# Performance work log

Measured on AMD Instinct MI355X. Metric: run time of the kernel, lower is better.

Reference implementation:

```python
import jax, jax.numpy as jnp
import numpy as np

B, T, C, H, N = 4, 2048, 1024, 16, 64
CHUNK = 256           # chunk_len
NBSWA = 2             # n_bswa_chunks
BSWA = CHUNK * NBSWA  # sliding window length
SSTATE = CHUNK        # kvm state slots (chunk_len * n_max_d_chunks)
SINK = 1              # sink_len
PARTIAL = 32          # rope_partial_dim
NEG = -1e30


def _ln(x, w, b, eps=1e-5):
    m = x.mean(-1, keepdims=True)
    v = jnp.mean((x - m) ** 2, -1, keepdims=True)
    return (x - m) * jax.lax.rsqrt(v + eps) * w + b


def _rope_tables():
    freq = (1.0 / 10000.0) ** np.linspace(0.0, 1.0, PARTIAL // 2, dtype=np.float32)
    freq = np.repeat(freq, 2)
    freq = np.concatenate([freq, np.zeros(N - PARTIAL, np.float32)])
    th = np.arange(T, dtype=np.float32)[:, None] * freq[None, :]
    cos = np.cos(th)
    sin = np.sin(th)
    sin[:, 1::2] *= -1.0
    return jnp.asarray(cos), jnp.asarray(sin)


def _rope(x, cos, sin):
    # pairwise flip (x0,x1)->(x1,x0)
    xf = x.reshape(*x.shape[:-1], N // 2, 2)[..., ::-1].reshape(x.shape)
    return cos[None, :, None, :] * x + sin[None, :, None, :] * xf


def _forward(residual, x, v1, x0, dx0,
             Wq, Wk, Wv, Wproj, Wkw,
             x_q, x_k, x_v, lamb,
             ln_q_w, ln_q_b, ln_k_w, ln_k_b, ln_dk_w, ln_dk_b, ln_res_w, ln_res_b,
             front_temp, state_temp):
    q = x @ Wq.T
    k = x @ Wk.T
    v = x @ Wv.T
    v = (1.0 - lamb) * v + lamb * v1  # value residual
    q = q.reshape(B, T, H, N)
    k = k.reshape(B, T, H, N)
    v = v.reshape(B, T, H, N)
    q = _ln(q, ln_q_w, ln_q_b)
    k = _ln(k, ln_k_w, ln_k_b)

    def shift(t):  # token shift (use_dkys=True variant)
        return jnp.concatenate([t[:, 0:1], t[:, :-1]], axis=1)

    q = q + x_q[None, None] * (shift(q) - q)
    k = k + x_k[None, None] * (shift(k) - k)
    v = v + x_v[None, None] * (shift(v) - v)

    cos, sin = _rope_tables()
    q = _rope(q, cos, sin)
    k = _rope(k, cos, sin)

    q = q.transpose(0, 2, 1, 3)  # [B,H,T,N]
    k = k.transpose(0, 2, 1, 3)
    v = v.transpose(0, 2, 1, 3)

    kw = jax.nn.sigmoid(jnp.einsum('btc,hc->bht', x, Wkw))[..., None]  # [B,H,T,1]
    st = state_temp.reshape(1, H, 1, 1)
    ft = front_temp.reshape(1, H, 1, 1)

    d_k = jnp.zeros((B, H, SSTATE, N), x.dtype)
    d_v = jnp.zeros((B, H, SSTATE, N), x.dtype)
    d_cnt = jnp.zeros((B, H, SSTATE, 1), x.dtype)
    scale = 1.0 / np.sqrt(N)
    outs = []
    for e in range(CHUNK, T + 1, CHUNK):  # fixed 8 chunks
        qb = e - CHUNK
        bb = max(0, e - BSWA)
        qc = q[:, :, qb:e]
        c_k = k[:, :, bb:bb + CHUNK]
        c_v = v[:, :, bb:bb + CHUNK]
        bk = k[:, :, bb:e]
        bv = v[:, :, bb:e]

        d_k_norm = _ln(d_k, ln_dk_w, ln_dk_b)
        d_vlen = d_cnt  # running count of accumulated c_v vectors per slot
        v_state = d_v / jnp.clip(jnp.linalg.norm(d_v, axis=-1, keepdims=True), 1e-12) * d_vlen
        k_star = jnp.concatenate([d_k_norm * st, bk * ft], axis=-2)
        v_star = jnp.concatenate([v_state, bv], axis=-2)

        qi = np.arange(qb, e)
        ki = np.arange(bb, e)
        mbias = np.where(ki[None, :] <= qi[:, None], 0.0, NEG).astype(np.float32)
        bias = jnp.asarray(np.concatenate([np.zeros((CHUNK, SSTATE), np.float32), mbias], axis=1))

        sc = jnp.einsum('bhqd,bhkd->bhqk', qc, k_star) * scale + bias
        out = jnp.einsum('bhqk,bhkd->bhqd', jax.nn.softmax(sc, axis=-1), v_star)
        outs.append(out)

        # state update: rope_zeroing on first PARTIAL channels, ln_d_k, nearest-slot scatter
        ck0 = jnp.concatenate([jnp.zeros_like(c_k[..., :PARTIAL]), c_k[..., PARTIAL:]], axis=-1)
        ck0 = _ln(ck0, ln_dk_w, ln_dk_b)
        sim = jnp.einsum('bhcd,bhsd->bhcs', ck0, d_k_norm)
        sim = sim.at[..., 0:SINK].set(NEG)
        kwc = kw[:, :, bb:bb + CHUNK]
        ck0 = ck0 * kwc
        cvw = c_v * kwc
        best = jnp.argmax(sim, axis=-1)                       # [B,H,CHUNK]
        oh = jax.nn.one_hot(best, SSTATE, dtype=x.dtype)      # [B,H,CHUNK,S]
        d_k = d_k + jnp.einsum('bhcs,bhcd->bhsd', oh, ck0)
        d_v = d_v + jnp.einsum('bhcs,bhcd->bhsd', oh, cvw)
        d_cnt = d_cnt + oh.sum(axis=2)[..., None]

    y = jnp.concatenate(outs, axis=2).transpose(0, 2, 1, 3).reshape(B, T, C)
    y = _ln(y, ln_res_w, ln_res_b)
    return residual + y @ Wproj.T


def setup_inputs() -> dict:
    key = jax.random.key(0)
    ks = jax.random.split(key, 12)
    f = lambda k, s, sc=1.0: jax.random.normal(k, s, dtype=jnp.float32) * sc
    return {
        'residual': f(ks[0], (B, T, C)),
        'x': f(ks[1], (B, T, C)),
        'v1': f(ks[2], (B, T, C)),
        'x0': f(ks[3], (B, T, C)),
        'dx0': f(ks[4], (B, T, C)),
        'token_ids': jax.random.randint(ks[5], (B, T), 0, 50257),
        'Wq': f(ks[6], (C, C), 0.02),
        'Wk': f(ks[7], (C, C), 0.02),
        'Wv': f(ks[8], (C, C), 0.02),
        'Wproj': f(ks[9], (C, C), 0.02),
        'Wkw': f(ks[10], (H, C), 0.02),
        'x_q': 0.5 * jnp.ones((H, N), jnp.float32),
        'x_k': 0.5 * jnp.ones((H, N), jnp.float32),
        'x_v': 0.5 * jnp.ones((H, N), jnp.float32),
        'lamb': jnp.float32(0.5),
        'ln_q_w': jnp.ones((N,), jnp.float32), 'ln_q_b': jnp.zeros((N,), jnp.float32),
        'ln_k_w': jnp.ones((N,), jnp.float32), 'ln_k_b': jnp.zeros((N,), jnp.float32),
        'ln_dk_w': jnp.ones((N,), jnp.float32), 'ln_dk_b': jnp.zeros((N,), jnp.float32),
        'ln_res_w': jnp.ones((C,), jnp.float32), 'ln_res_b': jnp.zeros((C,), jnp.float32),
        'front_temp': jnp.ones((H,), jnp.float32),
        'state_temp': jnp.ones((H,), jnp.float32),
    }


def reference(residual, x, v1, x0, dx0, token_ids,
              Wq, Wk, Wv, Wproj, Wkw, x_q, x_k, x_v, lamb,
              ln_q_w, ln_q_b, ln_k_w, ln_k_b, ln_dk_w, ln_dk_b, ln_res_w, ln_res_b,
              front_temp, state_temp):
    del token_ids  # unused in visible forward body
    return _forward(residual, x, v1, x0, dx0,
                    Wq, Wk, Wv, Wproj, Wkw,
                    x_q, x_k, x_v, lamb,
                    ln_q_w, ln_q_b, ln_k_w, ln_k_b, ln_dk_w, ln_dk_b, ln_res_w, ln_res_b,
                    front_temp, state_temp)
```

## Files before the change

kernel.cpp:

```cpp
#include <hip/hip_runtime.h>
#include <math.h>

#define Bq 4
#define Tq 2048
#define Cq 1024
#define Hq 16
#define Nq 64

typedef __attribute__((ext_vector_type(8))) short short8v;
typedef __attribute__((ext_vector_type(4))) float f32x4;

__device__ inline float waveSum(float v) {
#pragma unroll
  for (int o = 32; o; o >>= 1) v += __shfl_xor(v, o);
  return v;
}
__device__ inline unsigned short f2bf(float f) {
  unsigned u = __float_as_uint(f);
  unsigned r = (u + 0x7FFFu + ((u >> 16) & 1u)) >> 16;
  return (unsigned short)r;
}
__device__ inline float bf2f(unsigned short b) {
  return __uint_as_float(((unsigned)b) << 16);
}
// ... 123 lines not shown
      for (int j = 0; j < 4; ++j) {
        acc[i][j] = __builtin_amdgcn_mfma_f32_16x16x32_bf16(ah[i], bh[j], acc[i][j], 0, 0, 0);
        acc[i][j] = __builtin_amdgcn_mfma_f32_16x16x32_bf16(ah[i], bl[j], acc[i][j], 0, 0, 0);
        acc[i][j] = __builtin_amdgcn_mfma_f32_16x16x32_bf16(al[i], bh[j], acc[i][j], 0, 0, 0);
      }
  }

#pragma unroll
  for (int i = 0; i < 4; ++i)
#pragma unroll
    for (int j = 0; j < 4; ++j)
#pragma unroll
      for (int rg = 0; rg < 4; ++rg) {
        int m = m0 + wr * 64 + i * 16 + (l >> 4) * 4 + rg;
        int n = n0 + wc * 64 + j * 16 + (l & 15);
        int b = m >> 11, t = m & (Tq - 1);
        int h = n >> 6, nn = n & 63;
        dst[((((size_t)b * Hq + h) * Tq + t) << 6) | nn] = acc[i][j][rg];
      }
}

__global__ __launch_bounds__(256) void postproc(
    const float* __restrict__ src, float* __restrict__ dst,
    unsigned short* __restrict__ dst_bf,
    const float* __restrict__ lnw, const float* __restrict__ lnb,
    const float* __restrict__ xs_p, int doLNRope)
{
  const int w = threadIdx.x >> 6, lane = threadIdx.x & 63;
  const int row = blockIdx.x * 4 + w;
  const int t = row & (Tq - 1);
  const int h = (row >> 11) & (Hq - 1);
  const size_t base = (size_t)row << 6;
  const size_t pbase = (t > 0) ? base - 64 : base;
  float cur = src[base + lane];
  float prv = src[pbase + lane];
  if (doLNRope) {
    const float lw = lnw[lane], lb = lnb[lane];
    {
      float m = waveSum(cur) * (1.0f / 64.0f);
      float d = cur - m;
      float var = waveSum(d * d) * (1.0f / 64.0f);
      cur = d * rsqrtf(var + 1e-5f) * lw + lb;
    }
    {
      float m = waveSum(prv) * (1.0f / 64.0f);
      float d = prv - m;
      float var = waveSum(d * d) * (1.0f / 64.0f);
      prv = d * rsqrtf(var + 1e-5f) * lw + lb;
    }
  }
  const float xv = xs_p[h * 64 + lane];
  float val = cur + xv * (prv - cur);
  if (doLNRope) {
    float partner = __shfl_xor(val, 1);
    if (lane < 32) {
      int i = lane >> 1;
      float freq = (float)exp((double)i * (-log(10000.0) / 15.0));
      float th = (float)t * freq;
      float c = cosf(th), s = sinf(th);
      val = c * val + ((lane & 1) ? -s : s) * partner;
    }
  }
  if (dst) dst[base + lane] = val;
  if (dst_bf) dst_bf[base + lane] = f2bf(val);
}

__global__ __launch_bounds__(256) void kw_kernel(
    const float* __restrict__ x, const float* __restrict__ Wkw, float* __restrict__ out)
{
  const int bt = blockIdx.x;
  const int tid = threadIdx.x, w = tid >> 6, lane = tid & 63;
  __shared__ float xs[Cq];
  for (int i = tid; i < Cq; i += 256) xs[i] = x[(size_t)bt * Cq + i];
  __syncthreads();
  const int b = bt >> 11, t = bt & (Tq - 1);
  for (int h = w; h < Hq; h += 4) {
    float acc = 0.0f;
    for (int i = lane; i < Cq; i += 64) acc += xs[i] * Wkw[h * Cq + i];
    acc = waveSum(acc);
    if (lane == 0) out[((size_t)(b * Hq + h)) * Tq + t] = 1.0f / (1.0f + expf(-acc));
  }
}

__global__ __launch_bounds__(1024, 1) void state_evolve_kernel(
    const float* __restrict__ kf, const unsigned short* __restrict__ v_bf,
    const float* __restrict__ kwp,
    unsigned short* __restrict__ dkn_bf, unsigned short* __restrict__ vst_bf,
    float* __restrict__ cnt_snap,
    const float* __restrict__ lnw, const float* __restrict__ lnb)
{
  const int bh = blockIdx.x;
  const int tid = threadIdx.x;
  const int s = tid >> 2, qd = tid & 3;
  const int db = qd * 16;
  const size_t seq = (size_t)Tq * Nq;
  const float* kb_ = kf + (size_t)bh * seq;
  const unsigned short* vb_ = v_bf + (size_t)bh * seq;
  const float* kwb = kwp + (size_t)bh * Tq;

  __shared__ float dknT[32 * 260];
  __shared__ float ck0T[32 * 260];
  __shared__ unsigned short VRow[256 * 72];
  __shared__ float Ps[256], Qs[256], aS[256], kwS[256];
  __shared__ float lwS[64], lbS[64];
  __shared__ int best[256];

  if (tid < 64) { lwS[tid] = lnw[tid]; lbS[tid] = lnb[tid]; }

  float dkReg[16], dvReg[16];
#pragma unroll
  for (int i = 0; i < 16; ++i) { dkReg[i] = 0.f; dvReg[i] = 0.f; }
  float cnt = 0.f;
  __syncthreads();

  for (int c = 0; c < 8; ++c) {
    const int e = c * 256 + 256;
    const int bb = (e - 512 > 0) ? (e - 512) : 0;

    {
      float sum = 0.f;
#pragma unroll
      for (int i = 0; i < 16; ++i) sum += dkReg[i];
      sum += __shfl_xor(sum, 1); sum += __shfl_xor(sum, 2);
      const float mean = sum * (1.0f / 64.0f);
      float sq = 0.f;
#pragma unroll
      for (int i = 0; i < 16; ++i) { float d = dkReg[i] - mean; sq += d * d; }
      sq += __shfl_xor(sq, 1); sq += __shfl_xor(sq, 2);
      const float rs = rsqrtf(sq * (1.0f / 64.0f) + 1e-5f);
      float kn[16];
#pragma unroll
      for (int i = 0; i < 16; ++i)
        kn[i] = (dkReg[i] - mean) * rs * lwS[db + i] + lbS[db + i];
      unsigned int pk[8];
#pragma unroll
      for (int i2 = 0; i2 < 8; ++i2)
        pk[i2] = (unsigned)f2bf(kn[2 * i2]) | ((unsigned)f2bf(kn[2 * i2 + 1]) << 16);
      unsigned short* kd = dkn_bf + (((size_t)bh * 8 + c) << 14) + s * 64 + db;
      *(uint4*)kd = make_uint4(pk[0], pk[1], pk[2], pk[3]);
      *(uint4*)(kd + 8) = make_uint4(pk[4], pk[5], pk[6], pk[7]);

      if (c > 0 && c < 7) {
        if (qd >= 2) {
#pragma unroll
          for (int i = 0; i < 16; ++i) dknT[(db - 32 + i) * 260 + s] = kn[i];
        } else {
          float pp = 0.f, qq = 0.f;
#pragma unroll
          for (int i = 0; i < 16; ++i) {
            pp += kn[i] * lwS[db + i];
            qq += kn[i] * lbS[db + i];
          }
          pp += __shfl_xor(pp, 1);
          qq += __shfl_xor(qq, 1);
          if (qd == 0) { Ps[s] = pp; Qs[s] = qq; }
        }
      }

      float sqv = 0.f;
#pragma unroll
      for (int i = 0; i < 16; ++i) sqv += dvReg[i] * dvReg[i];
      sqv += __shfl_xor(sqv, 1); sqv += __shfl_xor(sqv, 2);
      const float inrm = 1.0f / fmaxf(sqrtf(sqv), 1e-12f);
#pragma unroll
      for (int i2 = 0; i2 < 8; ++i2)
        pk[i2] = (unsigned)f2bf(dvReg[2 * i2] * inrm) |
                 ((unsigned)f2bf(dvReg[2 * i2 + 1] * inrm) << 16);
      unsigned short* vd = vst_bf + (((size_t)bh * 8 + c) << 14) + s * 64 + db;
      *(uint4*)vd = make_uint4(pk[0], pk[1], pk[2], pk[3]);
      *(uint4*)(vd + 8) = make_uint4(pk[4], pk[5], pk[6], pk[7]);
      if (qd == 0) cnt_snap[((size_t)bh * 8 + c) * 256 + s] = cnt;
    }

    if (c == 7) break;

    {
      float kv[16];
      if (qd >= 2) {
        const float* krow = kb_ + (size_t)(bb + s) * 64 + db;
#pragma unroll
        for (int i = 0; i < 16; i += 4) {
          float4 t4 = *(const float4*)(krow + i);
          kv[i] = t4.x; kv[i + 1] = t4.y; kv[i + 2] = t4.z; kv[i + 3] = t4.w;
        }
      } else {
#pragma unroll
        for (int i = 0; i < 16; ++i) kv[i] = 0.f;
      }
      float sum = 0.f;
#pragma unroll
      for (int i = 0; i < 16; ++i) sum += kv[i];
      sum += __shfl_xor(sum, 1); sum += __shfl_xor(sum, 2);
      const float mean = sum * (1.0f / 64.0f);
      float sq = 0.f;
#pragma unroll
      for (int i = 0; i < 16; ++i) { float d = kv[i] - mean; sq += d * d; }
      sq += __shfl_xor(sq, 1); sq += __shfl_xor(sq, 2);
      const float rs = rsqrtf(sq * (1.0f / 64.0f) + 1e-5f);
      if (qd >= 2) {
#pragma unroll
        for (int i = 0; i < 16; ++i)
          ck0T[(db - 32 + i) * 260 + s] =
              (kv[i] - mean) * rs * lwS[db + i] + lbS[db + i];
      }
      if (qd == 0) {
        aS[s] = (0.0f - mean) * rs;
        kwS[s] = kwb[bb + s];
      }
      const unsigned short* vsrc = vb_ + (size_t)(bb + s) * 64 + db;
      *(uint4*)&VRow[s * 72 + db] = *(const uint4*)vsrc;
      *(uint4*)&VRow[s * 72 + db + 8] = *(const uint4*)(vsrc + 8);
      if (c == 0 && tid < 256) best[tid] = 1;
    }
    __syncthreads();

    if (c > 0) {
      const int tx = tid & 31, ty = tid >> 5;
      const f32x4 pv0 = *(const f32x4*)&Ps[4 * tx];
      const f32x4 pv1 = *(const f32x4*)&Ps[128 + 4 * tx];
      const f32x4 qv0 = *(const f32x4*)&Qs[4 * tx];
      const f32x4 qv1 = *(const f32x4*)&Qs[128 + 4 * tx];
#pragma unroll
      for (int pass = 0; pass < 2; ++pass) {
        const int rc0 = pass * 128 + ty * 4;
        float a4[4];
#pragma unroll
        for (int i = 0; i < 4; ++i) a4[i] = aS[rc0 + i];
        float acc[4][8];
#pragma unroll
        for (int i = 0; i < 4; ++i)
#pragma unroll
          for (int j = 0; j < 4; ++j) {
            acc[i][j] = a4[i] * pv0[j] + qv0[j];
            acc[i][j + 4] = a4[i] * pv1[j] + qv1[j];
          }
#pragma unroll 4
        for (int k = 0; k < 32; ++k) {
          f32x4 av = *(const f32x4*)&ck0T[k * 260 + rc0];
          f32x4 b0 = *(const f32x4*)&dknT[k * 260 + 4 * tx];
          f32x4 b1 = *(const f32x4*)&dknT[k * 260 + 128 + 4 * tx];
#pragma unroll
          for (int i = 0; i < 4; ++i)
#pragma unroll
            for (int j = 0; j < 4; ++j) {
              acc[i][j] += av[i] * b0[j];
              acc[i][j + 4] += av[i] * b1[j];
            }
        }
#pragma unroll
        for (int i = 0; i < 4; ++i) {
          float bvv = -3.0e38f;
          int bi = 1 << 30;
#pragma unroll
          for (int j = 0; j < 8; ++j) {
            int s2 = (j < 4) ? (4 * tx + j) : (128 + 4 * tx + (j - 4));
            float v = acc[i][j];
            if (s2 == 0) v = -1.0e30f;
            if (v > bvv || (v == bvv && s2 < bi)) { bvv = v; bi = s2; }
          }
#pragma unroll
          for (int o = 16; o; o >>= 1) {
            float ov = __shfl_xor(bvv, o);
            int oi = __shfl_xor(bi, o);
            if (ov > bvv || (ov == bvv && oi < bi)) { bvv = ov; bi = oi; }
          }
          if (tx == 0) best[rc0 + i] = bi;
        }
      }
      __syncthreads();
    }

    {
      int cadd = 0;
      for (int rc = 0; rc < 256; ++rc) {
        if (best[rc] == s) {
          const float kwv = kwS[rc];
          if (qd < 2) {
            const float a = aS[rc];
#pragma unroll
            for (int i = 0; i < 16; ++i)
              dkReg[i] += (a * lwS[db + i] + lbS[db + i]) * kwv;
          } else {
#pragma unroll
            for (int i = 0; i < 16; ++i)
              dkReg[i] += ck0T[(db - 32 + i) * 260 + rc] * kwv;
          }
          const uint4 u0 = *(const uint4*)&VRow[rc * 72 + db];
          const uint4 u1 = *(const uint4*)&VRow[rc * 72 + db + 8];
          const unsigned uu[8] = {u0.x, u0.y, u0.z, u0.w, u1.x, u1.y, u1.z, u1.w};
#pragma unroll
          for (int i2 = 0; i2 < 8; ++i2) {
            dvReg[2 * i2] += __uint_as_float((uu[i2] & 0xFFFFu) << 16) * kwv;
            dvReg[2 * i2 + 1] += __uint_as_float(uu[i2] & 0xFFFF0000u) * kwv;
          }
          ++cadd;
        }
      }
      cnt += (float)cadd;
    }
    __syncthreads();
  }
}

__global__ __launch_bounds__(256, 2) void attn_mfma_kernel(
    const unsigned short* __restrict__ q_bf, const unsigned short* __restrict__ k_bf,
    const unsigned short* __restrict__ v_bf,
    const unsigned short* __restrict__ dkn_bf, const unsigned short* __restrict__ vst_bf,
    const float* __restrict__ cnt_snap, float* __restrict__ y,
    const float* __restrict__ ftp, const float* __restrict__ stp)
{
  const int blk = blockIdx.x;
  const int bh = blk >> 4;
  const int c = (blk >> 1) & 7;
  const int half = blk & 1;
  const int h = bh & (Hq - 1);
  const int tid = threadIdx.x;
  const int w = tid >> 6, l = tid & 63;
  const int g = l >> 4, n = l & 15;
  const int rows0 = c * 256 + half * 128 + w * 32;
  const int e = c * 256 + 256;
  const int bb = (e - 512 > 0) ? (e - 512) : 0;
  const int nwt = (e - bb) >> 6;
  const float stsc = stp[h] * 0.125f, ftsc = ftp[h] * 0.125f;
  const size_t seq = (size_t)Tq * Nq;

  __shared__ unsigned short Ks[64 * 72];
  __shared__ unsigned short VTs[64 * 72];
  __shared__ unsigned short Ps[4][32 * 72];
  __shared__ float wts[64];

  short8v qf[2][2];
#pragma unroll
  for (int mt = 0; mt < 2; ++mt)
#pragma unroll
    for (int kh = 0; kh < 2; ++kh)
      qf[mt][kh] = *(const short8v*)(q_bf + (size_t)bh * seq +
                                     (size_t)(rows0 + mt * 16 + n) * 64 + kh * 32 + g * 8);

  f32x4 oacc[2][4];
#pragma unroll
  for (int mt = 0; mt < 2; ++mt)
#pragma unroll
    for (int dt = 0; dt < 4; ++dt) oacc[mt][dt] = (f32x4){0.f, 0.f, 0.f, 0.f};
  float rowM[2][4], rowL[2][4];
#pragma unroll
  for (int mt = 0; mt < 2; ++mt)
#pragma unroll
    for (int r = 0; r < 4; ++r) { rowM[mt][r] = -1.0e30f; rowL[mt][r] = 0.f; }

  const int nkt = 4 + nwt;
  for (int kt = 0; kt < nkt; ++kt) {
    const bool isState = kt < 4;
    const int t0 = isState ? kt * 64 : bb + (kt - 4) * 64;
    const unsigned short* ksrc = isState
        ? dkn_bf + (((size_t)bh * 8 + c) << 14) + (size_t)t0 * 64
        : k_bf + (size_t)bh * seq + (size_t)t0 * 64;
    const unsigned short* vsrc = isState
        ? vst_bf + (((size_t)bh * 8 + c) << 14) + (size_t)t0 * 64
        : v_bf + (size_t)bh * seq + (size_t)t0 * 64;

    __syncthreads();
    {
      const int row = tid >> 2, q4 = tid & 3;
      const unsigned short* src = ksrc + row * 64 + q4 * 16;
      *(uint4*)&Ks[row * 72 + q4 * 16] = *(const uint4*)src;
      *(uint4*)&Ks[row * 72 + q4 * 16 + 8] = *(const uint4*)(src + 8);
      const unsigned short* vs = vsrc + row * 64 + q4 * 16;
#pragma unroll
      for (int i = 0; i < 16; ++i) VTs[(q4 * 16 + i) * 72 + row] = vs[i];
      if (tid < 64)
        wts[tid] = isState ? cnt_snap[((size_t)bh * 8 + c) * 256 + kt * 64 + tid] : 1.0f;
    }
    __syncthreads();

    f32x4 sacc[2][4];
#pragma unroll
    for (int mt = 0; mt < 2; ++mt)
#pragma unroll
      for (int nt = 0; nt < 4; ++nt) sacc[mt][nt] = (f32x4){0.f, 0.f, 0.f, 0.f};
#pragma unroll
    for (int nt = 0; nt < 4; ++nt) {
      short8v kf0 = *(const short8v*)&Ks[(nt * 16 + n) * 72 + g * 8];
      short8v kf1 = *(const short8v*)&Ks[(nt * 16 + n) * 72 + 32 + g * 8];
#pragma unroll
      for (int mt = 0; mt < 2; ++mt) {
        sacc[mt][nt] = __builtin_amdgcn_mfma_f32_16x16x32_bf16(qf[mt][0], kf0, sacc[mt][nt], 0, 0, 0);
        sacc[mt][nt] = __builtin_amdgcn_mfma_f32_16x16x32_bf16(qf[mt][1], kf1, sacc[mt][nt], 0, 0, 0);
      }
    }

    const float scale = isState ? stsc : ftsc;
    float wt_n[4];
#pragma unroll
    for (int nt = 0; nt < 4; ++nt) wt_n[nt] = wts[nt * 16 + n];

#pragma unroll
    for (int mt = 0; mt < 2; ++mt) {
#pragma unroll
      for (int r = 0; r < 4; ++r) {
        float sv[4];
#pragma unroll
        for (int nt = 0; nt < 4; ++nt) {
          float s = sacc[mt][nt][r] * scale;
          if (!isState) {
            int qi = rows0 + mt * 16 + g * 4 + r;
            int kj = t0 + nt * 16 + n;
            if (kj > qi) s = -1.0e30f;
          }
          sv[nt] = s;
        }
        float tmax = fmaxf(fmaxf(sv[0], sv[1]), fmaxf(sv[2], sv[3]));
        tmax = fmaxf(tmax, __shfl_xor(tmax, 1));
        tmax = fmaxf(tmax, __shfl_xor(tmax, 2));
        tmax = fmaxf(tmax, __shfl_xor(tmax, 4));
        tmax = fmaxf(tmax, __shfl_xor(tmax, 8));
        const float Mold = rowM[mt][r];
        const float Mnew = fmaxf(Mold, tmax);
        const float al = __expf(Mold - Mnew);
        rowM[mt][r] = Mnew;
        float p[4], ts = 0.f;
#pragma unroll
        for (int nt = 0; nt < 4; ++nt) { p[nt] = __expf(sv[nt] - Mnew); ts += p[nt]; }
        ts += __shfl_xor(ts, 1);
        ts += __shfl_xor(ts, 2);
        ts += __shfl_xor(ts, 4);
        ts += __shfl_xor(ts, 8);
        rowL[mt][r] = rowL[mt][r] * al + ts;
#pragma unroll
        for (int dt = 0; dt < 4; ++dt) oacc[mt][dt][r] *= al;
        const int prow = (mt * 16 + g * 4 + r) * 72;
#pragma unroll
        for (int nt = 0; nt < 4; ++nt)
          Ps[w][prow + nt * 16 + n] = f2bf(p[nt] * wt_n[nt]);
      }
    }

    short8v pf[2][2];
#pragma unroll
    for (int mt = 0; mt < 2; ++mt)
#pragma unroll
      for (int jh = 0; jh < 2; ++jh)
        pf[mt][jh] = *(const short8v*)&Ps[w][(mt * 16 + n) * 72 + jh * 32 + g * 8];
#pragma unroll
    for (int dt = 0; dt < 4; ++dt) {
      short8v vf0 = *(const short8v*)&VTs[(dt * 16 + n) * 72 + g * 8];
      short8v vf1 = *(const short8v*)&VTs[(dt * 16 + n) * 72 + 32 + g * 8];
#pragma unroll
      for (int mt = 0; mt < 2; ++mt) {
        oacc[mt][dt] = __builtin_amdgcn_mfma_f32_16x16x32_bf16(pf[mt][0], vf0, oacc[mt][dt], 0, 0, 0);
        oacc[mt][dt] = __builtin_amdgcn_mfma_f32_16x16x32_bf16(pf[mt][1], vf1, oacc[mt][dt], 0, 0, 0);
      }
    }
  }

#pragma unroll
  for (int mt = 0; mt < 2; ++mt) {
#pragma unroll
    for (int r = 0; r < 4; ++r) {
      const float inv = 1.0f / rowL[mt][r];
      const int row = rows0 + mt * 16 + g * 4 + r;
#pragma unroll
      for (int dt = 0; dt < 4; ++dt)
        y[(size_t)bh * seq + (size_t)row * 64 + dt * 16 + n] = oacc[mt][dt][r] * inv;
    }
  }
}

__global__ __launch_bounds__(256) void final_ln(
    const float* __restrict__ y, const float* __restrict__ lnw,
    const float* __restrict__ lnb, unsigned short* __restrict__ dst)
{
  const int bt = blockIdx.x;
  const int b = bt >> 11, t = bt & (Tq - 1);
  const int tid = threadIdx.x, w = tid >> 6, lane = tid & 63;
  __shared__ float red[8];
  float v[4];
  float s = 0.0f;
#pragma unroll
  for (int i = 0; i < 4; ++i) {
    int c = tid + (i << 8);
    int h = c >> 6, n = c & 63;
    v[i] = y[((((size_t)b * Hq + h) * Tq + t) << 6) + n];
    s += v[i];
  }
  s = waveSum(s);
  if (lane == 0) red[w] = s;
  __syncthreads();
  const float mean = (red[0] + red[1] + red[2] + red[3]) * (1.0f / 1024.0f);
  float s2 = 0.0f;
#pragma unroll
  for (int i = 0; i < 4; ++i) { float d = v[i] - mean; s2 += d * d; }
  s2 = waveSum(s2);
  if (lane == 0) red[4 + w] = s2;
  __syncthreads();
  const float var = (red[4] + red[5] + red[6] + red[7]) * (1.0f / 1024.0f);
  const float rs = rsqrtf(var + 1e-5f);
#pragma unroll
  for (int i = 0; i < 4; ++i) {
    int c = tid + (i << 8);
    dst[(size_t)bt * Cq + c] = f2bf((v[i] - mean) * rs * lnw[c] + lnb[c]);
  }
}

extern "C" void kernel_launch(void* const* d_in, const int* in_sizes, int n_in,
                              void* d_out, int out_size, void* d_ws, size_t ws_size,
                              hipStream_t stream)
{
  (void)in_sizes; (void)n_in; (void)out_size; (void)ws_size;
  const float* residual = (const float*)d_in[0];
  const float* x        = (const float*)d_in[1];
  const float* v1       = (const float*)d_in[2];
  const float* Wq       = (const float*)d_in[6];
  const float* Wk       = (const float*)d_in[7];
  const float* Wv       = (const float*)d_in[8];
  const float* Wproj    = (const float*)d_in[9];
  const float* Wkw      = (const float*)d_in[10];
  const float* x_q      = (const float*)d_in[11];
  const float* x_k      = (const float*)d_in[12];
  const float* x_v      = (const float*)d_in[13];
  const float* lamb     = (const float*)d_in[14];
  const float* ln_q_w   = (const float*)d_in[15];
  const float* ln_q_b   = (const float*)d_in[16];
  const float* ln_k_w   = (const float*)d_in[17];
  const float* ln_k_b   = (const float*)d_in[18];
  const float* ln_dk_w  = (const float*)d_in[19];
  const float* ln_dk_b  = (const float*)d_in[20];
  const float* ln_res_w = (const float*)d_in[21];
  const float* ln_res_b = (const float*)d_in[22];
  const float* ftp      = (const float*)d_in[23];
  const float* stp      = (const float*)d_in[24];

  float* ws = (float*)d_ws;
  const size_t SZ = (size_t)Bq * Hq * Tq * Nq;
  float* q_raw = ws;
  float* ybuf  = ws;
  float* k_raw = ws + SZ;
  unsigned short* vst_bf = (unsigned short*)(ws + SZ);
  float* cnt_snap = ws + SZ + SZ / 2;
  float* v_mix = ws + 2 * SZ;
  unsigned short* ylnb_bf = (unsigned short*)(ws + 2 * SZ);
  float* k_fin = ws + 3 * SZ;
  unsigned short* q_bf = (unsigned short*)(ws + 4 * SZ);
  unsigned short* x_lo = q_bf;
  unsigned short* k_bf = q_bf + SZ;
  unsigned short* wk_hi = k_bf;
  unsigned short* wk_lo = wk_hi + (1u << 20);
  unsigned short* v_bf = (unsigned short*)(ws + 5 * SZ);
  unsigned short* xb   = v_bf + SZ;
  unsigned short* dkn_bf = xb;
  unsigned short* wqb = (unsigned short*)(ws + 6 * SZ);
  unsigned short* wvb = wqb + (1u << 20);
  unsigned short* wpb = wvb + (1u << 20);
  float* kwbuf = ws + 6 * SZ + ((3u << 20) >> 1);

  dim3 gb(256);
  dim3 ggb(64, 8);

  hipLaunchKernelGGL(f32_to_bf16_hilo_kernel, dim3((int)(SZ / 4 / 256)), gb, 0, stream,
                     x, xb, x_lo, (int)(SZ / 4));
  hipLaunchKernelGGL(f32_to_bf16_hilo_kernel, dim3(1024), gb, 0, stream,
                     Wk, wk_hi, wk_lo, 262144);
  hipLaunchKernelGGL(f32_to_bf16_kernel, dim3(1024), gb, 0, stream, Wq, wqb, 262144);
  hipLaunchKernelGGL(f32_to_bf16_kernel, dim3(1024), gb, 0, stream, Wv, wvb, 262144);
  hipLaunchKernelGGL(f32_to_bf16_kernel, dim3(1024), gb, 0, stream, Wproj, wpb, 262144);

  hipLaunchKernelGGL(gemm_bf16, ggb, gb, 0, stream, xb, wqb, q_raw, (const float*)nullptr, lamb, 1);
  hipLaunchKernelGGL(gemm_bf16_split, ggb, gb, 0, stream, xb, x_lo, wk_hi, wk_lo, k_raw);
  hipLaunchKernelGGL(gemm_bf16, ggb, gb, 0, stream, xb, wvb, v_mix, v1, lamb, 2);
  hipLaunchKernelGGL(kw_kernel, dim3(Bq * Tq), gb, 0, stream, x, Wkw, kwbuf);

  const int rows = Bq * Hq * Tq;
  hipLaunchKernelGGL(postproc, dim3(rows / 4), gb, 0, stream, q_raw, (float*)nullptr, q_bf, ln_q_w, ln_q_b, x_q, 1);
  hipLaunchKernelGGL(postproc, dim3(rows / 4), gb, 0, stream, k_raw, k_fin, k_bf, ln_k_w, ln_k_b, x_k, 1);
  hipLaunchKernelGGL(postproc, dim3(rows / 4), gb, 0, stream, v_mix, (float*)nullptr, v_bf,
                     (const float*)nullptr, (const float*)nullptr, x_v, 0);

  hipLaunchKernelGGL(state_evolve_kernel, dim3(Bq * Hq), dim3(1024), 0, stream,
                     k_fin, v_bf, kwbuf, dkn_bf, vst_bf, cnt_snap, ln_dk_w, ln_dk_b);

  hipLaunchKernelGGL(attn_mfma_kernel, dim3(Bq * Hq * 16), gb, 0, stream,
                     q_bf, k_bf, v_bf, dkn_bf, vst_bf, cnt_snap, ybuf, ftp, stp);

  hipLaunchKernelGGL(final_ln, dim3(Bq * Tq), gb, 0, stream, ybuf, ln_res_w, ln_res_b, ylnb_bf);
  hipLaunchKernelGGL(gemm_bf16, ggb, gb, 0, stream, ylnb_bf, wpb, (float*)d_out, residual, lamb, 3);
}
```

Baseline: 1.405 ms.

## Overlap sequential state evolution with windowed attention in one heterogeneous kernel

Merges the state-evolution kernel and the sliding-window part of attention into a single launch. The first 64 blocks run the serial per-head state update, while the remaining blocks compute unnormalised window attention and write partial outputs plus row max and sum. A separate merge kernel then does only the state-slot attention and combines the two softmax partials. The state scatter loop also gains per-slot counts so rows with no assignments exit early. This hides the long single-block-per-head state kernel behind window attention, at the cost of extra partial-output traffic and a merge step.

```diff
diff --git a/kernel.cpp b/kernel.cpp
--- a/kernel.cpp
+++ b/kernel.cpp
@@ -229,232 +229,370 @@
   }
 }
 
-__global__ __launch_bounds__(1024, 1) void state_evolve_kernel(
+union MegaSmem {
+  struct {
+    float dknT[32 * 260];
+    float ck0T[32 * 260];
+    unsigned short VRow[256 * 72];
+    float Ps[256], Qs[256], aS[256], kwS[256];
+    float lwS[64], lbS[64];
+    int best[256];
+    int cntS[256];
+  } st;
+  struct {
+    unsigned short Ks[64 * 72];
+    unsigned short VTs[64 * 72];
+    unsigned short Ps[16][16 * 72];
+  } at;
+};
+
+__global__ __launch_bounds__(1024, 1) void mega_state_window_kernel(
     const float* __restrict__ kf, const unsigned short* __restrict__ v_bf,
     const float* __restrict__ kwp,
     unsigned short* __restrict__ dkn_bf, unsigned short* __restrict__ vst_bf,
     float* __restrict__ cnt_snap,
-    const float* __restrict__ lnw, const float* __restrict__ lnb)
-{
-  const int bh = blockIdx.x;
+    const float* __restrict__ lnw, const float* __restrict__ lnb,
+    const unsigned short* __restrict__ q_bf, const unsigned short* __restrict__ k_bf,
+    float* __restrict__ ow, float* __restrict__ mlw, const float* __restrict__ ftp)
+{
+  __shared__ MegaSmem sm;
   const int tid = threadIdx.x;
-  const int s = tid >> 2, qd = tid & 3;
-  const int db = qd * 16;
   const size_t seq = (size_t)Tq * Nq;
-  const float* kb_ = kf + (size_t)bh * seq;
-  const unsigned short* vb_ = v_bf + (size_t)bh * seq;
-  const float* kwb = kwp + (size_t)bh * Tq;
-
-  __shared__ float dknT[32 * 260];
-  __shared__ float ck0T[32 * 260];
-  __shared__ unsigned short VRow[256 * 72];
-  __shared__ float Ps[256], Qs[256], aS[256], kwS[256];
-  __shared__ float lwS[64], lbS[64];
-  __shared__ int best[256];
-
-  if (tid < 64) { lwS[tid] = lnw[tid]; lbS[tid] = lnb[tid]; }
-
-  float dkReg[16], dvReg[16];
-#pragma unroll
-  for (int i = 0; i < 16; ++i) { dkReg[i] = 0.f; dvReg[i] = 0.f; }
-  float cnt = 0.f;
-  __syncthreads();
-
-  for (int c = 0; c < 8; ++c) {
+
+  if (blockIdx.x < 64) {
+    auto& S = sm.st;
+    const int bh = blockIdx.x;
+    const int s = tid >> 2, qd = tid & 3;
+    const int db = qd * 16;
+    const float* kb_ = kf + (size_t)bh * seq;
+    const unsigned short* vb_ = v_bf + (size_t)bh * seq;
+    const float* kwb = kwp + (size_t)bh * Tq;
+
+    if (tid < 64) { S.lwS[tid] = lnw[tid]; S.lbS[tid] = lnb[tid]; }
+
+    float dkReg[16], dvReg[16];
+#pragma unroll
+    for (int i = 0; i < 16; ++i) { dkReg[i] = 0.f; dvReg[i] = 0.f; }
+    float cnt = 0.f;
+    __syncthreads();
+
+    for (int c = 0; c < 8; ++c) {
+      const int e = c * 256 + 256;
+      const int bb = (e - 512 > 0) ? (e - 512) : 0;
+
+      {
+        float sum = 0.f;
+#pragma unroll
+        for (int i = 0; i < 16; ++i) sum += dkReg[i];
+        sum += __shfl_xor(sum, 1); sum += __shfl_xor(sum, 2);
+        const float mean = sum * (1.0f / 64.0f);
+        float sq = 0.f;
+#pragma unroll
+        for (int i = 0; i < 16; ++i) { float d = dkReg[i] - mean; sq += d * d; }
+        sq += __shfl_xor(sq, 1); sq += __shfl_xor(sq, 2);
+        const float rs = rsqrtf(sq * (1.0f / 64.0f) + 1e-5f);
+        float kn[16];
+#pragma unroll
+        for (int i = 0; i < 16; ++i)
+          kn[i] = (dkReg[i] - mean) * rs * S.lwS[db + i] + S.lbS[db + i];
+        unsigned int pk[8];
+#pragma unroll
+        for (int i2 = 0; i2 < 8; ++i2)
+          pk[i2] = (unsigned)f2bf(kn[2 * i2]) | ((unsigned)f2bf(kn[2 * i2 + 1]) << 16);
+        unsigned short* kd = dkn_bf + (((size_t)bh * 8 + c) << 14) + s * 64 + db;
+        *(uint4*)kd = make_uint4(pk[0], pk[1], pk[2], pk[3]);
+        *(uint4*)(kd + 8) = make_uint4(pk[4], pk[5], pk[6], pk[7]);
+
+        if (c > 0 && c < 7) {
+          if (qd >= 2) {
+#pragma unroll
+            for (int i = 0; i < 16; ++i) S.dknT[(db - 32 + i) * 260 + s] = kn[i];
+          } else {
+            float pp = 0.f, qq = 0.f;
+#pragma unroll
+            for (int i = 0; i < 16; ++i) {
+              pp += kn[i] * S.lwS[db + i];
+              qq += kn[i] * S.lbS[db + i];
+            }
+            pp += __shfl_xor(pp, 1);
+            qq += __shfl_xor(qq, 1);
+            if (qd == 0) { S.Ps[s] = pp; S.Qs[s] = qq; }
+          }
+        }
+
+        float sqv = 0.f;
+#pragma unroll
+        for (int i = 0; i < 16; ++i) sqv += dvReg[i] * dvReg[i];
+        sqv += __shfl_xor(sqv, 1); sqv += __shfl_xor(sqv, 2);
+        const float inrm = 1.0f / fmaxf(sqrtf(sqv), 1e-12f);
+#pragma unroll
+        for (int i2 = 0; i2 < 8; ++i2)
+          pk[i2] = (unsigned)f2bf(dvReg[2 * i2] * inrm) |
+                   ((unsigned)f2bf(dvReg[2 * i2 + 1] * inrm) << 16);
+        unsigned short* vd = vst_bf + (((size_t)bh * 8 + c) << 14) + s * 64 + db;
+        *(uint4*)vd = make_uint4(pk[0], pk[1], pk[2], pk[3]);
+        *(uint4*)(vd + 8) = make_uint4(pk[4], pk[5], pk[6], pk[7]);
+        if (qd == 0) cnt_snap[((size_t)bh * 8 + c) * 256 + s] = cnt;
+      }
+
+      if (c == 7) break;
+
+      {
+        float kv[16];
+        if (qd >= 2) {
+          const float* krow = kb_ + (size_t)(bb + s) * 64 + db;
+#pragma unroll
+          for (int i = 0; i < 16; i += 4) {
+            float4 t4 = *(const float4*)(krow + i);
+            kv[i] = t4.x; kv[i + 1] = t4.y; kv[i + 2] = t4.z; kv[i + 3] = t4.w;
+          }
+        } else {
+#pragma unroll
+          for (int i = 0; i < 16; ++i) kv[i] = 0.f;
+        }
+        float sum = 0.f;
+#pragma unroll
+        for (int i = 0; i < 16; ++i) sum += kv[i];
+        sum += __shfl_xor(sum, 1); sum += __shfl_xor(sum, 2);
+        const float mean = sum * (1.0f / 64.0f);
+        float sq = 0.f;
+#pragma unroll
+        for (int i = 0; i < 16; ++i) { float d = kv[i] - mean; sq += d * d; }
+        sq += __shfl_xor(sq, 1); sq += __shfl_xor(sq, 2);
+        const float rs = rsqrtf(sq * (1.0f / 64.0f) + 1e-5f);
+        if (qd >= 2) {
+#pragma unroll
+          for (int i = 0; i < 16; ++i)
+            S.ck0T[(db - 32 + i) * 260 + s] =
+                (kv[i] - mean) * rs * S.lwS[db + i] + S.lbS[db + i];
+        }
+        if (qd == 0) {
+          S.aS[s] = (0.0f - mean) * rs;
+          S.kwS[s] = kwb[bb + s];
+        }
+        const unsigned short* vsrc = vb_ + (size_t)(bb + s) * 64 + db;
+        *(uint4*)&S.VRow[s * 72 + db] = *(const uint4*)vsrc;
+        *(uint4*)&S.VRow[s * 72 + db + 8] = *(const uint4*)(vsrc + 8);
+        if (c == 0) {
+          if (tid < 256) { S.best[tid] = 1; S.cntS[tid] = (tid == 1) ? 256 : 0; }
+        } else {
+          if (tid < 256) S.cntS[tid] = 0;
+        }
+      }
+      __syncthreads();
+
+      if (c > 0) {
+        const int tx = tid & 31, ty = tid >> 5;
+        const f32x4 pv0 = *(const f32x4*)&S.Ps[4 * tx];
+        const f32x4 pv1 = *(const f32x4*)&S.Ps[128 + 4 * tx];
+        const f32x4 qv0 = *(const f32x4*)&S.Qs[4 * tx];
+        const f32x4 qv1 = *(const f32x4*)&S.Qs[128 + 4 * tx];
+#pragma unroll
+        for (int pass = 0; pass < 2; ++pass) {
+          const int rc0 = pass * 128 + ty * 4;
+          float a4[4];
+#pragma unroll
+          for (int i = 0; i < 4; ++i) a4[i] = S.aS[rc0 + i];
+          float acc[4][8];
+#pragma unroll
+          for (int i = 0; i < 4; ++i)
+#pragma unroll
+            for (int j = 0; j < 4; ++j) {
+              acc[i][j] = a4[i] * pv0[j] + qv0[j];
+              acc[i][j + 4] = a4[i] * pv1[j] + qv1[j];
+            }
+#pragma unroll 4
+          for (int k = 0; k < 32; ++k) {
+            f32x4 av = *(const f32x4*)&S.ck0T[k * 260 + rc0];
+            f32x4 b0 = *(const f32x4*)&S.dknT[k * 260 + 4 * tx];
+            f32x4 b1 = *(const f32x4*)&S.dknT[k * 260 + 128 + 4 * tx];
+#pragma unroll
+            for (int i = 0; i < 4; ++i)
+#pragma unroll
+              for (int j = 0; j < 4; ++j) {
+                acc[i][j] += av[i] * b0[j];
+                acc[i][j + 4] += av[i] * b1[j];
+              }
+          }
+#pragma unroll
+          for (int i = 0; i < 4; ++i) {
+            float bvv = -3.0e38f;
+            int bi = 1 << 30;
+#pragma unroll
+            for (int j = 0; j < 8; ++j) {
+              int s2 = (j < 4) ? (4 * tx + j) : (128 + 4 * tx + (j - 4));
+              float v = acc[i][j];
+              if (s2 == 0) v = -1.0e30f;
+              if (v > bvv || (v == bvv && s2 < bi)) { bvv = v; bi = s2; }
+            }
+#pragma unroll
+            for (int o = 16; o; o >>= 1) {
+              float ov = __shfl_xor(bvv, o);
+              int oi = __shfl_xor(bi, o);
+              if (ov > bvv || (ov == bvv && oi < bi)) { bvv = ov; bi = oi; }
+            }
+            if (tx == 0) {
+              S.best[rc0 + i] = bi;
+              atomicAdd(&S.cntS[bi], 1);
+            }
+          }
+        }
+      }
+      __syncthreads();
+
+      {
+        const int need = S.cntS[s];
+        if (need) {
+          int found = 0;
+          for (int rc = 0; rc < 256 && found < need; ++rc) {
+            if (S.best[rc] == s) {
+              const float kwv = S.kwS[rc];
+              if (qd < 2) {
+                const float a = S.aS[rc];
+#pragma unroll
+                for (int i = 0; i < 16; ++i)
+                  dkReg[i] += (a * S.lwS[db + i] + S.lbS[db + i]) * kwv;
+              } else {
+#pragma unroll
+                for (int i = 0; i < 16; ++i)
+                  dkReg[i] += S.ck0T[(db - 32 + i) * 260 + rc] * kwv;
+              }
+              const uint4 u0 = *(const uint4*)&S.VRow[rc * 72 + db];
+              const uint4 u1 = *(const uint4*)&S.VRow[rc * 72 + db + 8];
+              const unsigned uu[8] = {u0.x, u0.y, u0.z, u0.w, u1.x, u1.y, u1.z, u1.w};
+#pragma unroll
+              for (int i2 = 0; i2 < 8; ++i2) {
+                dvReg[2 * i2] += __uint_as_float((uu[i2] & 0xFFFFu) << 16) * kwv;
+                dvReg[2 * i2 + 1] += __uint_as_float(uu[i2] & 0xFFFF0000u) * kwv;
+              }
+              ++found;
+            }
+          }
+          cnt += (float)need;
+        }
+      }
+      __syncthreads();
+    }
+  } else {
+    auto& A = sm.at;
+    const int wb = blockIdx.x - 64;
+    const int bh = wb >> 3;
+    const int c = wb & 7;
+    const int h = bh & (Hq - 1);
+    const int w16 = tid >> 6, l = tid & 63;
+    const int g = l >> 4, n = l & 15;
+    const int rows0 = c * 256 + w16 * 16;
     const int e = c * 256 + 256;
     const int bb = (e - 512 > 0) ? (e - 512) : 0;
-
-    {
-      float sum = 0.f;
-#pragma unroll
-      for (int i = 0; i < 16; ++i) sum += dkReg[i];
-      sum += __shfl_xor(sum, 1); sum += __shfl_xor(sum, 2);
-      const float mean = sum * (1.0f / 64.0f);
-      float sq = 0.f;
-#pragma unroll
-      for (int i = 0; i < 16; ++i) { float d = dkReg[i] - mean; sq += d * d; }
-      sq += __shfl_xor(sq, 1); sq += __shfl_xor(sq, 2);
-      const float rs = rsqrtf(sq * (1.0f / 64.0f) + 1e-5f);
-      float kn[16];
-#pragma unroll
-      for (int i = 0; i < 16; ++i)
-        kn[i] = (dkReg[i] - mean) * rs * lwS[db + i] + lbS[db + i];
-      unsigned int pk[8];
-#pragma unroll
-      for (int i2 = 0; i2 < 8; ++i2)
-        pk[i2] = (unsigned)f2bf(kn[2 * i2]) | ((unsigned)f2bf(kn[2 * i2 + 1]) << 16);
-      unsigned short* kd = dkn_bf + (((size_t)bh * 8 + c) << 14) + s * 64 + db;
-      *(uint4*)kd = make_uint4(pk[0], pk[1], pk[2], pk[3]);
-      *(uint4*)(kd + 8) = make_uint4(pk[4], pk[5], pk[6], pk[7]);
-
-      if (c > 0 && c < 7) {
-        if (qd >= 2) {
-#pragma unroll
-          for (int i = 0; i < 16; ++i) dknT[(db - 32 + i) * 260 + s] = kn[i];
-        } else {
-          float pp = 0.f, qq = 0.f;
-#pragma unroll
-          for (int i = 0; i < 16; ++i) {
-            pp += kn[i] * lwS[db + i];
-            qq += kn[i] * lbS[db + i];
-          }
-          pp += __shfl_xor(pp, 1);
-          qq += __shfl_xor(qq, 1);
-          if (qd == 0) { Ps[s] = pp; Qs[s] = qq; }
+    const int nwt = (e - bb) >> 6;
+    const float ftsc = ftp[h] * 0.125f;
+
+    short8v qf[2];
+#pragma unroll
+    for (int kh = 0; kh < 2; ++kh)
+      qf[kh] = *(const short8v*)(q_bf + (size_t)bh * seq +
+                                 (size_t)(rows0 + n) * 64 + kh * 32 + g * 8);
+
+    f32x4 oacc[4];
+#pragma unroll
+    for (int dt = 0; dt < 4; ++dt) oacc[dt] = (f32x4){0.f, 0.f, 0.f, 0.f};
+    float rowM[4], rowL[4];
+#pragma unroll
+    for (int r = 0; r < 4; ++r) { rowM[r] = -1.0e30f; rowL[r] = 0.f; }
+
+    for (int kt = 0; kt < nwt; ++kt) {
+      const int t0 = bb + kt * 64;
+      const unsigned short* ksrc = k_bf + (size_t)bh * seq + (size_t)t0 * 64;
+      const unsigned short* vsrc = v_bf + (size_t)bh * seq + (size_t)t0 * 64;
+      __syncthreads();
+      {
+        const int row = tid >> 4, q16 = tid & 15;
+        *(uint2*)&A.Ks[row * 72 + q16 * 4] = *(const uint2*)(ksrc + row * 64 + q16 * 4);
+        const unsigned short* vs = vsrc + row * 64 + q16 * 4;
+#pragma unroll
+        for (int i = 0; i < 4; ++i) A.VTs[(q16 * 4 + i) * 72 + row] = vs[i];
+      }
+      __syncthreads();
+
+      f32x4 sacc[4];
+#pragma unroll
+      for (int nt = 0; nt < 4; ++nt) sacc[nt] = (f32x4){0.f, 0.f, 0.f, 0.f};
+#pragma unroll
+      for (int nt = 0; nt < 4; ++nt) {
+        short8v kf0 = *(const short8v*)&A.Ks[(nt * 16 + n) * 72 + g * 8];
+        short8v kf1 = *(const short8v*)&A.Ks[(nt * 16 + n) * 72 + 32 + g * 8];
+        sacc[nt] = __builtin_amdgcn_mfma_f32_16x16x32_bf16(qf[0], kf0, sacc[nt], 0, 0, 0);
+        sacc[nt] = __builtin_amdgcn_mfma_f32_16x16x32_bf16(qf[1], kf1, sacc[nt], 0, 0, 0);
+      }
+
+#pragma unroll
+      for (int r = 0; r < 4; ++r) {
+        const int qi = rows0 + g * 4 + r;
+        float sv[4];
+#pragma unroll
+        for (int nt = 0; nt < 4; ++nt) {
+          float s = sacc[nt][r] * ftsc;
+          int kj = t0 + nt * 16 + n;
+          if (kj > qi) s = -1.0e30f;
+          sv[nt] = s;
         }
-      }
-
-      float sqv = 0.f;
-#pragma unroll
-      for (int i = 0; i < 16; ++i) sqv += dvReg[i] * dvReg[i];
-      sqv += __shfl_xor(sqv, 1); sqv += __shfl_xor(sqv, 2);
-      const float inrm = 1.0f / fmaxf(sqrtf(sqv), 1e-12f);
-#pragma unroll
-      for (int i2 = 0; i2 < 8; ++i2)
-        pk[i2] = (unsigned)f2bf(dvReg[2 * i2] * inrm) |
-                 ((unsigned)f2bf(dvReg[2 * i2 + 1] * inrm) << 16);
-      unsigned short* vd = vst_bf + (((size_t)bh * 8 + c) << 14) + s * 64 + db;
-      *(uint4*)vd = make_uint4(pk[0], pk[1], pk[2], pk[3]);
-      *(uint4*)(vd + 8) = make_uint4(pk[4], pk[5], pk[6], pk[7]);
-      if (qd == 0) cnt_snap[((size_t)bh * 8 + c) * 256 + s] = cnt;
-    }
-
-    if (c == 7) break;
-
-    {
-      float kv[16];
-      if (qd >= 2) {
-        const float* krow = kb_ + (size_t)(bb + s) * 64 + db;
-#pragma unroll
-        for (int i = 0; i < 16; i += 4) {
-          float4 t4 = *(const float4*)(krow + i);
-          kv[i] = t4.x; kv[i + 1] = t4.y; kv[i + 2] = t4.z; kv[i + 3] = t4.w;
-        }
-      } else {
-#pragma unroll
-        for (int i = 0; i < 16; ++i) kv[i] = 0.f;
-      }
-      float sum = 0.f;
-#pragma unroll
-      for (int i = 0; i < 16; ++i) sum += kv[i];
-      sum += __shfl_xor(sum, 1); sum += __shfl_xor(sum, 2);
-      const float mean = sum * (1.0f / 64.0f);
-      float sq = 0.f;
-#pragma unroll
-      for (int i = 0; i < 16; ++i) { float d = kv[i] - mean; sq += d * d; }
-      sq += __shfl_xor(sq, 1); sq += __shfl_xor(sq, 2);
-      const float rs = rsqrtf(sq * (1.0f / 64.0f) + 1e-5f);
-      if (qd >= 2) {
-#pragma unroll
-        for (int i = 0; i < 16; ++i)
-          ck0T[(db - 32 + i) * 260 + s] =
-              (kv[i] - mean) * rs * lwS[db + i] + lbS[db + i];
-      }
-      if (qd == 0) {
-        aS[s] = (0.0f - mean) * rs;
-        kwS[s] = kwb[bb + s];
-      }
-      const unsigned short* vsrc = vb_ + (size_t)(bb + s) * 64 + db;
-      *(uint4*)&VRow[s * 72 + db] = *(const uint4*)vsrc;
-      *(uint4*)&VRow[s * 72 + db + 8] = *(const uint4*)(vsrc + 8);
-      if (c == 0 && tid < 256) best[tid] = 1;
-    }
-    __syncthreads();
-
-    if (c > 0) {
-      const int tx = tid & 31, ty = tid >> 5;
-      const f32x4 pv0 = *(const f32x4*)&Ps[4 * tx];
-      const f32x4 pv1 = *(const f32x4*)&Ps[128 + 4 * tx];
-      const f32x4 qv0 = *(const f32x4*)&Qs[4 * tx];
-      const f32x4 qv1 = *(const f32x4*)&Qs[128 + 4 * tx];
-#pragma unroll
-      for (int pass = 0; pass < 2; ++pass) {
-        const int rc0 = pass * 128 + ty * 4;
-        float a4[4];
-#pragma unroll
-        for (int i = 0; i < 4; ++i) a4[i] = aS[rc0 + i];
-        float acc[4][8];
-#pragma unroll
-        for (int i = 0; i < 4; ++i)
-#pragma unroll
-          for (int j = 0; j < 4; ++j) {
-            acc[i][j] = a4[i] * pv0[j] + qv0[j];
-            acc[i][j + 4] = a4[i] * pv1[j] + qv1[j];
-          }
-#pragma unroll 4
-        for (int k = 0; k < 32; ++k) {
-          f32x4 av = *(const f32x4*)&ck0T[k * 260 + rc0];
-          f32x4 b0 = *(const f32x4*)&dknT[k * 260 + 4 * tx];
-          f32x4 b1 = *(const f32x4*)&dknT[k * 260 + 128 + 4 * tx];
-#pragma unroll
-          for (int i = 0; i < 4; ++i)
-#pragma unroll
-            for (int j = 0; j < 4; ++j) {
-              acc[i][j] += av[i] * b0[j];
-              acc[i][j + 4] += av[i] * b1[j];
-            }
-        }
-#pragma unroll
-        for (int i = 0; i < 4; ++i) {
-          float bvv = -3.0e38f;
-          int bi = 1 << 30;
-#pragma unroll
-          for (int j = 0; j < 8; ++j) {
-            int s2 = (j < 4) ? (4 * tx + j) : (128 + 4 * tx + (j - 4));
-            float v = acc[i][j];
-            if (s2 == 0) v = -1.0e30f;
-            if (v > bvv || (v == bvv && s2 < bi)) { bvv = v; bi = s2; }
-          }
-#pragma unroll
-          for (int o = 16; o; o >>= 1) {
-            float ov = __shfl_xor(bvv, o);
-            int oi = __shfl_xor(bi, o);
-            if (ov > bvv || (ov == bvv && oi < bi)) { bvv = ov; bi = oi; }
-          }
-          if (tx == 0) best[rc0 + i] = bi;
-        }
-      }
-      __syncthreads();
-    }
-
-    {
-      int cadd = 0;
-      for (int rc = 0; rc < 256; ++rc) {
-        if (best[rc] == s) {
-          const float kwv = kwS[rc];
-          if (qd < 2) {
-            const float a = aS[rc];
-#pragma unroll
-            for (int i = 0; i < 16; ++i)
-              dkReg[i] += (a * lwS[db + i] + lbS[db + i]) * kwv;
-          } else {
-#pragma unroll
-            for (int i = 0; i < 16; ++i)
-              dkReg[i] += ck0T[(db - 32 + i) * 260 + rc] * kwv;
-          }
-          const uint4 u0 = *(const uint4*)&VRow[rc * 72 + db];
-          const uint4 u1 = *(const uint4*)&VRow[rc * 72 + db + 8];
-          const unsigned uu[8] = {u0.x, u0.y, u0.z, u0.w, u1.x, u1.y, u1.z, u1.w};
-#pragma unroll
-          for (int i2 = 0; i2 < 8; ++i2) {
-            dvReg[2 * i2] += __uint_as_float((uu[i2] & 0xFFFFu) << 16) * kwv;
-            dvReg[2 * i2 + 1] += __uint_as_float(uu[i2] & 0xFFFF0000u) * kwv;
-          }
-          ++cadd;
-        }
-      }
-      cnt += (float)cadd;
-    }
-    __syncthreads();
-  }
-}
-
-__global__ __launch_bounds__(256, 2) void attn_mfma_kernel(
-    const unsigned short* __restrict__ q_bf, const unsigned short* __restrict__ k_bf,
-    const unsigned short* __restrict__ v_bf,
+        float tmax = fmaxf(fmaxf(sv[0], sv[1]), fmaxf(sv[2], sv[3]));
+        tmax = fmaxf(tmax, __shfl_xor(tmax, 1));
+        tmax = fmaxf(tmax, __shfl_xor(tmax, 2));
+        tmax = fmaxf(tmax, __shfl_xor(tmax, 4));
+        tmax = fmaxf(tmax, __shfl_xor(tmax, 8));
+        const float Mold = rowM[r];
+        const float Mnew = fmaxf(Mold, tmax);
+        const float al = __expf(Mold - Mnew);
+        rowM[r] = Mnew;
+        float p[4], ts = 0.f;
+#pragma unroll
+        for (int nt = 0; nt < 4; ++nt) { p[nt] = __expf(sv[nt] - Mnew); ts += p[nt]; }
+        ts += __shfl_xor(ts, 1);
+        ts += __shfl_xor(ts, 2);
+        ts += __shfl_xor(ts, 4);
+        ts += __shfl_xor(ts, 8);
+        rowL[r] = rowL[r] * al + ts;
+#pragma unroll
+        for (int dt = 0; dt < 4; ++dt) oacc[dt][r] *= al;
+        const int prow = (g * 4 + r) * 72;
+#pragma unroll
+        for (int nt = 0; nt < 4; ++nt)
+          A.Ps[w16][prow + nt * 16 + n] = f2bf(p[nt]);
+      }
+
+      short8v pf[2];
+#pragma unroll
+      for (int jh = 0; jh < 2; ++jh)
+        pf[jh] = *(const short8v*)&A.Ps[w16][n * 72 + jh * 32 + g * 8];
+#pragma unroll
+      for (int dt = 0; dt < 4; ++dt) {
+        short8v vf0 = *(const short8v*)&A.VTs[(dt * 16 + n) * 72 + g * 8];
+        short8v vf1 = *(const short8v*)&A.VTs[(dt * 16 + n) * 72 + 32 + g * 8];
+        oacc[dt] = __builtin_amdgcn_mfma_f32_16x16x32_bf16(pf[0], vf0, oacc[dt], 0, 0, 0);
+        oacc[dt] = __builtin_amdgcn_mfma_f32_16x16x32_bf16(pf[1], vf1, oacc[dt], 0, 0, 0);
+      }
+    }
+
+#pragma unroll
+    for (int r = 0; r < 4; ++r) {
+      const int row = rows0 + g * 4 + r;
+      if (n == 0) {
+        mlw[((size_t)bh * Tq + row) * 2] = rowM[r];
+        mlw[((size_t)bh * Tq + row) * 2 + 1] = rowL[r];
+      }
+#pragma unroll
+      for (int dt = 0; dt < 4; ++dt)
+        ow[(size_t)bh * seq + (size_t)row * 64 + dt * 16 + n] = oacc[dt][r];
+    }
+  }
+}
+
+__global__ __launch_bounds__(256, 2) void attn_state_merge_kernel(
+    const unsigned short* __restrict__ q_bf,
     const unsigned short* __restrict__ dkn_bf, const unsigned short* __restrict__ vst_bf,
     const float* __restrict__ cnt_snap, float* __restrict__ y,
-    const float* __restrict__ ftp, const float* __restrict__ stp)
+    const float* __restrict__ mlw, const float* __restrict__ stp)
 {
   const int blk = blockIdx.x;
   const int bh = blk >> 4;
@@ -465,10 +603,7 @@
   const int w = tid >> 6, l = tid & 63;
   const int g = l >> 4, n = l & 15;
   const int rows0 = c * 256 + half * 128 + w * 32;
-  const int e = c * 256 + 256;
-  const int bb = (e - 512 > 0) ? (e - 512) : 0;
-  const int nwt = (e - bb) >> 6;
-  const float stsc = stp[h] * 0.125f, ftsc = ftp[h] * 0.125f;
+  const float stsc = stp[h] * 0.125f;
   const size_t seq = (size_t)Tq * Nq;
 
   __shared__ unsigned short Ks[64 * 72];
@@ -495,16 +630,10 @@
 #pragma unroll
     for (int r = 0; r < 4; ++r) { rowM[mt][r] = -1.0e30f; rowL[mt][r] = 0.f; }
 
-  const int nkt = 4 + nwt;
-  for (int kt = 0; kt < nkt; ++kt) {
-    const bool isState = kt < 4;
-    const int t0 = isState ? kt * 64 : bb + (kt - 4) * 64;
-    const unsigned short* ksrc = isState
-        ? dkn_bf + (((size_t)bh * 8 + c) << 14) + (size_t)t0 * 64
-        : k_bf + (size_t)bh * seq + (size_t)t0 * 64;
-    const unsigned short* vsrc = isState
-        ? vst_bf + (((size_t)bh * 8 + c) << 14) + (size_t)t0 * 64
-        : v_bf + (size_t)bh * seq + (size_t)t0 * 64;
+  for (int kt = 0; kt < 4; ++kt) {
+    const int t0 = kt * 64;
+    const unsigned short* ksrc = dkn_bf + (((size_t)bh * 8 + c) << 14) + (size_t)t0 * 64;
+    const unsigned short* vsrc = vst_bf + (((size_t)bh * 8 + c) << 14) + (size_t)t0 * 64;
 
     __syncthreads();
     {
@@ -516,7 +645,7 @@
 #pragma unroll
       for (int i = 0; i < 16; ++i) VTs[(q4 * 16 + i) * 72 + row] = vs[i];
       if (tid < 64)
-        wts[tid] = isState ? cnt_snap[((size_t)bh * 8 + c) * 256 + kt * 64 + tid] : 1.0f;
+        wts[tid] = cnt_snap[((size_t)bh * 8 + c) * 256 + kt * 64 + tid];
     }
     __syncthreads();
 
@@ -536,7 +665,6 @@
       }
     }
 
-    const float scale = isState ? stsc : ftsc;
     float wt_n[4];
 #pragma unroll
     for (int nt = 0; nt < 4; ++nt) wt_n[nt] = wts[nt * 16 + n];
@@ -547,15 +675,7 @@
       for (int r = 0; r < 4; ++r) {
         float sv[4];
 #pragma unroll
-        for (int nt = 0; nt < 4; ++nt) {
-          float s = sacc[mt][nt][r] * scale;
-          if (!isState) {
-            int qi = rows0 + mt * 16 + g * 4 + r;
-            int kj = t0 + nt * 16 + n;
-            if (kj > qi) s = -1.0e30f;
-          }
-          sv[nt] = s;
-        }
+        for (int nt = 0; nt < 4; ++nt) sv[nt] = sacc[mt][nt][r] * stsc;
         float tmax = fmaxf(fmaxf(sv[0], sv[1]), fmaxf(sv[2], sv[3]));
         tmax = fmaxf(tmax, __shfl_xor(tmax, 1));
         tmax = fmaxf(tmax, __shfl_xor(tmax, 2));
@@ -604,11 +724,19 @@
   for (int mt = 0; mt < 2; ++mt) {
 #pragma unroll
     for (int r = 0; r < 4; ++r) {
-      const float inv = 1.0f / rowL[mt][r];
       const int row = rows0 + mt * 16 + g * 4 + r;
-#pragma unroll
-      for (int dt = 0; dt < 4; ++dt)
-        y[(size_t)bh * seq + (size_t)row * 64 + dt * 16 + n] = oacc[mt][dt][r] * inv;
+      const float mw_ = mlw[((size_t)bh * Tq + row) * 2];
+      const float lw_ = mlw[((size_t)bh * Tq + row) * 2 + 1];
+      const float mm = fmaxf(rowM[mt][r], mw_);
+      const float es = __expf(rowM[mt][r] - mm);
+      const float ew = __expf(mw_ - mm);
+      const float inv = 1.0f / (rowL[mt][r] * es + lw_ * ew);
+#pragma unroll
+      for (int dt = 0; dt < 4; ++dt) {
+        const size_t idx = (size_t)bh * seq + (size_t)row * 64 + dt * 16 + n;
+        const float ov = y[idx];
+        y[idx] = (oacc[mt][dt][r] * es + ov * ew) * inv;
+      }
     }
   }
 }
@@ -699,6 +827,7 @@
   unsigned short* wvb = wqb + (1u << 20);
   unsigned short* wpb = wvb + (1u << 20);
   float* kwbuf = ws + 6 * SZ + ((3u << 20) >> 1);
+  float* mlw = kwbuf + (size_t)Bq * Hq * Tq;
 
   dim3 gb(256);
   dim3 ggb(64, 8);
@@ -722,11 +851,12 @@
   hipLaunchKernelGGL(postproc, dim3(rows / 4), gb, 0, stream, v_mix, (float*)nullptr, v_bf,
                      (const float*)nullptr, (const float*)nullptr, x_v, 0);
 
-  hipLaunchKernelGGL(state_evolve_kernel, dim3(Bq * Hq), dim3(1024), 0, stream,
-                     k_fin, v_bf, kwbuf, dkn_bf, vst_bf, cnt_snap, ln_dk_w, ln_dk_b);
-
-  hipLaunchKernelGGL(attn_mfma_kernel, dim3(Bq * Hq * 16), gb, 0, stream,
-                     q_bf, k_bf, v_bf, dkn_bf, vst_bf, cnt_snap, ybuf, ftp, stp);
+  hipLaunchKernelGGL(mega_state_window_kernel, dim3(64 + Bq * Hq * 8), dim3(1024), 0, stream,
+                     k_fin, v_bf, kwbuf, dkn_bf, vst_bf, cnt_snap, ln_dk_w, ln_dk_b,
+                     q_bf, k_bf, ybuf, mlw, ftp);
+
+  hipLaunchKernelGGL(attn_state_merge_kernel, dim3(Bq * Hq * 16), gb, 0, stream,
+                     q_bf, dkn_bf, vst_bf, cnt_snap, ybuf, mlw, stp);
 
   hipLaunchKernelGGL(final_ln, dim3(Bq * Tq), gb, 0, stream, ybuf, ln_res_w, ln_res_b, ylnb_bf);
   hipLaunchKernelGGL(gemm_bf16, ggb, gb, 0, stream, ylnb_bf, wpb, (float*)d_out, residual, lamb, 3);
```

New measurement: 1.963 ms. +39.7%, slower.
